# Optimization experiments

Measured on AMD Instinct MI355X. Metric: run time of the kernel, lower is better.

Reference implementation:

```python
import jax, jax.numpy as jnp
import numpy as np

N_HEADS = 8
HEAD_D = 64


def setup_inputs() -> dict:
    key = jax.random.key(0)
    ks = jax.random.split(key, 7)
    b, ds, dc = 4, 4096, 256
    ls, lc = 512, 512
    inner = N_HEADS * HEAD_D  # 512
    out_dim = 512
    data = jax.random.normal(ks[0], (b, ds, dc), dtype=jnp.float32)
    latent = jax.random.normal(ks[1], (b, ls, lc), dtype=jnp.float32)
    # torch nn.Linear weights are [out_features, in_features]
    Wq = jax.random.normal(ks[2], (inner, lc), dtype=jnp.float32) * (lc ** -0.5)
    Wk = jax.random.normal(ks[3], (inner, dc), dtype=jnp.float32) * (dc ** -0.5)
    Wv = jax.random.normal(ks[4], (inner, dc), dtype=jnp.float32) * (dc ** -0.5)
    Wo = jax.random.normal(ks[5], (out_dim, inner), dtype=jnp.float32) * (inner ** -0.5)
    bo = jax.random.normal(ks[6], (out_dim,), dtype=jnp.float32) * 0.02
    return {"data": data, "latent": latent, "Wq": Wq, "Wk": Wk, "Wv": Wv, "Wo": Wo, "bo": bo}


def reference(data, latent, Wq, Wk, Wv, Wo, bo):
    b, ds, _ = data.shape
    ls = latent.shape[1]
    scale = HEAD_D ** -0.5
    # projections, split into heads
    Q = (latent @ Wq.T).reshape(b, ls, N_HEADS, HEAD_D)  # [b,ls,h,d]
    K = (data @ Wk.T).reshape(b, ds, N_HEADS, HEAD_D)    # [b,ds,h,d]
    V = (data @ Wv.T).reshape(b, ds, N_HEADS, HEAD_D)
    # logits [b, ds, ls, h]; original broadcasts then sums over head_d -> einsum
    logits = jnp.einsum('blhd,bshd->bslh', Q, K) * scale
    # softmax over key axis (dim 1 = ds), matching attn_logits.softmax(1)
    attn = jax.nn.softmax(logits, axis=1)
    # weighted sum over keys: [b, ls, h, d] -> [b, ls, inner]
    out = jnp.einsum('bshd,bslh->blhd', V, attn).reshape(b, ls, N_HEADS * HEAD_D)
    # output Linear (dropout is identity in eval)
    return out @ Wo.T + bo
```

## Files before the change

kernel.cpp:

```cpp
#include <hip/hip_runtime.h>

typedef __bf16 bf16;
typedef __bf16 bf16x8 __attribute__((ext_vector_type(8)));
typedef float  f32x4  __attribute__((ext_vector_type(4)));


__device__ __forceinline__ bf16x8 cvt8(float4 a, float4 b) {
    bf16x8 r;
    r[0] = (bf16)a.x; r[1] = (bf16)a.y; r[2] = (bf16)a.z; r[3] = (bf16)a.w;
    r[4] = (bf16)b.x; r[5] = (bf16)b.y; r[6] = (bf16)b.z; r[7] = (bf16)b.w;
    return r;
}

#define LDT 136
__global__ __launch_bounds__(256) void proj_kvq(
    const float* __restrict__ data, const float* __restrict__ latent,
    const float* __restrict__ Wk, const float* __restrict__ Wv, const float* __restrict__ Wq,
    bf16* __restrict__ K_b, bf16* __restrict__ Vt_b, bf16* __restrict__ Q_b)
{
    __shared__ __align__(16) bf16 arena[128 * LDT];

    const int bx = blockIdx.x;
    const int tid = threadIdx.x;
    const int wave = tid >> 6, lane = tid & 63;
    const int wm = wave >> 1, wn = wave & 1;
    const int l15 = lane & 15, quad = lane >> 4;
    const int rowA = tid >> 2;
    const int c8 = (tid & 3) * 8;

    if (bx >= 64) {
        const int t = bx - 64;
        const int m0 = (t & 127) * 128, n0 = (t >> 7) * 128;
        bf16* As  = arena;
        bf16* Bks = arena + 4096;
        bf16* Bvs = arena + 8192;

        const float* Ar0 = data + (size_t)(m0 + rowA) * 256 + c8;
        const float* Ar1 = Ar0 + 64 * 256;
        const float* Kr0 = Wk + (size_t)(n0 + rowA) * 256 + c8;
        const float* Kr1 = Kr0 + 64 * 256;
        const float* Vr0 = Wv + (size_t)(n0 + rowA) * 256 + c8;
        const float* Vr1 = Vr0 + 64 * 256;

        f32x4 accK[4][4] = {}, accV[4][4] = {};
        float4 a00,a01,a10,a11, k00,k01,k10,k11, v00,v01,v10,v11;

#define LOADF(k) do { \
        a00 = *(const float4*)(Ar0 + (k)); a01 = *(const float4*)(Ar0 + (k) + 4); \
        a10 = *(const float4*)(Ar1 + (k)); a11 = *(const float4*)(Ar1 + (k) + 4); \
        k00 = *(const float4*)(Kr0 + (k)); k01 = *(const float4*)(Kr0 + (k) + 4); \
        k10 = *(const float4*)(Kr1 + (k)); k11 = *(const float4*)(Kr1 + (k) + 4); \
        v00 = *(const float4*)(Vr0 + (k)); v01 = *(const float4*)(Vr0 + (k) + 4); \
        v10 = *(const float4*)(Vr1 + (k)); v11 = *(const float4*)(Vr1 + (k) + 4); \
    } while (0)

        LOADF(0);
        for (int k0 = 0; k0 < 256; k0 += 32) {
            __syncthreads();
            *(bf16x8*)(As + (size_t)tid * 8)         = cvt8(a00, a01);
            *(bf16x8*)(As + 2048 + (size_t)tid * 8)  = cvt8(a10, a11);
            *(bf16x8*)(Bks + (size_t)tid * 8)        = cvt8(k00, k01);
            *(bf16x8*)(Bks + 2048 + (size_t)tid * 8) = cvt8(k10, k11);
            *(bf16x8*)(Bvs + (size_t)tid * 8)        = cvt8(v00, v01);
            *(bf16x8*)(Bvs + 2048 + (size_t)tid * 8) = cvt8(v10, v11);
            if (k0 + 32 < 256) LOADF(k0 + 32);
            __syncthreads();

            bf16x8 af[4];
            #pragma unroll
            for (int mt = 0; mt < 4; mt++)
                af[mt] = *(const bf16x8*)(As + (wm * 64 + mt * 16 + l15) * 32 + quad * 8);
            #pragma unroll
            for (int nt = 0; nt < 4; nt++) {
                bf16x8 bk = *(const bf16x8*)(Bks + (wn * 64 + nt * 16 + l15) * 32 + quad * 8);
                #pragma unroll
                for (int mt = 0; mt < 4; mt++)
                    accK[mt][nt] = __builtin_amdgcn_mfma_f32_16x16x32_bf16(af[mt], bk, accK[mt][nt], 0, 0, 0);
            }
            #pragma unroll
            for (int nt = 0; nt < 4; nt++) {
                bf16x8 bv = *(const bf16x8*)(Bvs + (wn * 64 + nt * 16 + l15) * 32 + quad * 8);
                #pragma unroll
                for (int mt = 0; mt < 4; mt++)
                    accV[mt][nt] = __builtin_amdgcn_mfma_f32_16x16x32_bf16(af[mt], bv, accV[mt][nt], 0, 0, 0);
            }
        }
#undef LOADF

        __syncthreads();
        #pragma unroll
        for (int mt = 0; mt < 4; mt++)
            #pragma unroll
            for (int nt = 0; nt < 4; nt++)
                #pragma unroll
                for (int r = 0; r < 4; r++) {
                    int ml = wm * 64 + mt * 16 + quad * 4 + r;
                    int nl = wn * 64 + nt * 16 + l15;
                    arena[ml * LDT + nl] = (bf16)accK[mt][nt][r];
                }
        __syncthreads();
        #pragma unroll
        for (int c = 0; c < 8; c++) {
            int idx = c * 256 + tid;
            int row = idx >> 4, col = (idx & 15) * 8;
            bf16x8 vv = *(const bf16x8*)(arena + row * LDT + col);
            int m = m0 + row, n = n0 + col;
            *(bf16x8*)(K_b + (size_t)((m >> 12) * 8 + (n >> 6)) * 262144 + (m & 4095) * 64 + (n & 63)) = vv;
        }
        __syncthreads();
        #pragma unroll
        for (int mt = 0; mt < 4; mt++)
            #pragma unroll
            for (int nt = 0; nt < 4; nt++)
                #pragma unroll
                for (int r = 0; r < 4; r++) {
                    int ml = wm * 64 + mt * 16 + quad * 4 + r;
                    int nl = wn * 64 + nt * 16 + l15;
                    arena[nl * LDT + ml] = (bf16)accV[mt][nt][r];
                }
        __syncthreads();
        #pragma unroll
        for (int c = 0; c < 8; c++) {
            int idx = c * 256 + tid;
            int row = idx >> 4, col = (idx & 15) * 8;
            bf16x8 vv = *(const bf16x8*)(arena + row * LDT + col);
            int d = n0 + row, s = m0 + col;
            *(bf16x8*)(Vt_b + (size_t)((s >> 12) * 8 + (d >> 6)) * 262144 + (d & 63) * 4096 + (s & 4095)) = vv;
        }
    } else {
        const int m0 = (bx & 15) * 128, n0 = (bx >> 4) * 128;
        bf16* As = arena;
        bf16* Bs = arena + 4096;

        const float* Ar0 = latent + (size_t)(m0 + rowA) * 512 + c8;
        const float* Ar1 = Ar0 + 64 * 512;
        const float* Br0 = Wq + (size_t)(n0 + rowA) * 512 + c8;
        const float* Br1 = Br0 + 64 * 512;

        f32x4 acc[4][4] = {};
        float4 a00, a01, a10, a11, b00, b01, b10, b11;

#define LOADQ(k) do { \
        a00 = *(const float4*)(Ar0 + (k));  a01 = *(const float4*)(Ar0 + (k) + 4); \
        a10 = *(const float4*)(Ar1 + (k));  a11 = *(const float4*)(Ar1 + (k) + 4); \
        b00 = *(const float4*)(Br0 + (k));  b01 = *(const float4*)(Br0 + (k) + 4); \
        b10 = *(const float4*)(Br1 + (k));  b11 = *(const float4*)(Br1 + (k) + 4); \
    } while (0)

        LOADQ(0);
        for (int k0 = 0; k0 < 512; k0 += 32) {
            __syncthreads();
            *(bf16x8*)(As + (size_t)tid * 8)        = cvt8(a00, a01);
            *(bf16x8*)(As + 2048 + (size_t)tid * 8) = cvt8(a10, a11);
            *(bf16x8*)(Bs + (size_t)tid * 8)        = cvt8(b00, b01);
            *(bf16x8*)(Bs + 2048 + (size_t)tid * 8) = cvt8(b10, b11);
            if (k0 + 32 < 512) LOADQ(k0 + 32);
            __syncthreads();

            bf16x8 af[4], bfr[4];
            #pragma unroll
            for (int mt = 0; mt < 4; mt++)
                af[mt] = *(const bf16x8*)(As + (wm * 64 + mt * 16 + l15) * 32 + quad * 8);
            #pragma unroll
            for (int nt = 0; nt < 4; nt++)
                bfr[nt] = *(const bf16x8*)(Bs + (wn * 64 + nt * 16 + l15) * 32 + quad * 8);
            #pragma unroll
            for (int mt = 0; mt < 4; mt++)
                #pragma unroll
                for (int nt = 0; nt < 4; nt++)
                    acc[mt][nt] = __builtin_amdgcn_mfma_f32_16x16x32_bf16(af[mt], bfr[nt], acc[mt][nt], 0, 0, 0);
        }
#undef LOADQ

        __syncthreads();
        #pragma unroll
        for (int mt = 0; mt < 4; mt++)
            #pragma unroll
            for (int nt = 0; nt < 4; nt++)
                #pragma unroll
                for (int r = 0; r < 4; r++) {
                    int ml = wm * 64 + mt * 16 + quad * 4 + r;
                    int nl = wn * 64 + nt * 16 + l15;
                    arena[ml * LDT + nl] = (bf16)acc[mt][nt][r];
                }
        __syncthreads();
        #pragma unroll
        for (int c = 0; c < 8; c++) {
            int idx = c * 256 + tid;
            int row = idx >> 4, col = (idx & 15) * 8;
            bf16x8 vv = *(const bf16x8*)(arena + row * LDT + col);
            int m = m0 + row, n = n0 + col;
            *(bf16x8*)(Q_b + (size_t)((m >> 9) * 8 + (n >> 6)) * 32768 + (m & 511) * 64 + (n & 63)) = vv;
        }
    }
}

#define LDK 72
__global__ __launch_bounds__(256) void flash_attn(
    const bf16* __restrict__ Q, const bf16* __restrict__ K,
    const bf16* __restrict__ Vt, float* __restrict__ Opart, float* __restrict__ lbuf)
{
    __shared__ bf16 Ks[64 * LDK];
    __shared__ bf16 Vs[64 * LDK];
    __shared__ bf16 Ps[4][16 * LDK];

    const int tid = threadIdx.x;
    const int bx = blockIdx.x;
    const int qt = bx >> 7;
    const int bh = (bx & 127) >> 2;
    const int ks = bx & 3;
    const int wave = tid >> 6, lane = tid & 63;
    const int l15 = lane & 15, quad = lane >> 4;

    const bf16* Qb = Q + (size_t)bh * 32768 + (size_t)(qt * 64 + wave * 16 + l15) * 64;
    bf16x8 aq[2];
    aq[0] = *(const bf16x8*)(Qb + quad * 8);
    aq[1] = *(const bf16x8*)(Qb + 32 + quad * 8);

    const bf16* Kb = K + (size_t)bh * 262144;
    const bf16* Vb = Vt + (size_t)bh * 262144;

    f32x4 oacc[4] = {};
    float lpart[4] = {0.f, 0.f, 0.f, 0.f};
    const float scale = 0.125f;

    const int i0 = tid, i1 = tid + 256;
    const int r0 = i0 >> 3, c0 = (i0 & 7) * 8;
    const int r1 = i1 >> 3, c1 = (i1 & 7) * 8;

    const int kstart = ks * 1024, kend = kstart + 1024;

    uint4 pk0 = *(const uint4*)(Kb + (size_t)(kstart + r0) * 64 + c0);
    uint4 pk1 = *(const uint4*)(Kb + (size_t)(kstart + r1) * 64 + c1);
    uint4 pv0 = *(const uint4*)(Vb + (size_t)r0 * 4096 + kstart + c0);
    uint4 pv1 = *(const uint4*)(Vb + (size_t)r1 * 4096 + kstart + c1);

    for (int key0 = kstart; key0 < kend; key0 += 64) {
        __syncthreads();
        *(uint4*)(Ks + r0 * LDK + c0) = pk0;
        *(uint4*)(Ks + r1 * LDK + c1) = pk1;
        *(uint4*)(Vs + r0 * LDK + c0) = pv0;
        *(uint4*)(Vs + r1 * LDK + c1) = pv1;
        if (key0 + 64 < kend) {
            pk0 = *(const uint4*)(Kb + (size_t)(key0 + 64 + r0) * 64 + c0);
            pk1 = *(const uint4*)(Kb + (size_t)(key0 + 64 + r1) * 64 + c1);
            pv0 = *(const uint4*)(Vb + (size_t)r0 * 4096 + key0 + 64 + c0);
            pv1 = *(const uint4*)(Vb + (size_t)r1 * 4096 + key0 + 64 + c1);
        }
        __syncthreads();

        float p[4][4];
        __builtin_amdgcn_s_setprio(1);
        #pragma unroll
        for (int nt = 0; nt < 4; nt++) {
            f32x4 z = {};
            #pragma unroll
            for (int kf = 0; kf < 2; kf++) {
                bf16x8 bk = *(const bf16x8*)(Ks + (nt * 16 + l15) * LDK + kf * 32 + quad * 8);
                z = __builtin_amdgcn_mfma_f32_16x16x32_bf16(aq[kf], bk, z, 0, 0, 0);
            }
            #pragma unroll
            for (int r = 0; r < 4; r++) {
                float e = __expf(z[r] * scale);
                p[r][nt] = e;
                lpart[r] += e;
            }
        }
        __builtin_amdgcn_s_setprio(0);

        #pragma unroll
        for (int r = 0; r < 4; r++)
            #pragma unroll
            for (int nt = 0; nt < 4; nt++)
                Ps[wave][(quad * 4 + r) * LDK + nt * 16 + l15] = (bf16)p[r][nt];

        bf16x8 ap[2];
        ap[0] = *(const bf16x8*)(&Ps[wave][l15 * LDK + quad * 8]);
        ap[1] = *(const bf16x8*)(&Ps[wave][l15 * LDK + 32 + quad * 8]);
        __builtin_amdgcn_s_setprio(1);
        #pragma unroll
        for (int dt = 0; dt < 4; dt++) {
            #pragma unroll
            for (int kf = 0; kf < 2; kf++) {
                bf16x8 bv = *(const bf16x8*)(Vs + (dt * 16 + l15) * LDK + kf * 32 + quad * 8);
                oacc[dt] = __builtin_amdgcn_mfma_f32_16x16x32_bf16(ap[kf], bv, oacc[dt], 0, 0, 0);
            }
        }
        __builtin_amdgcn_s_setprio(0);
    }

    #pragma unroll
    for (int r = 0; r < 4; r++) {
        #pragma unroll
        for (int off = 1; off < 16; off <<= 1) lpart[r] += __shfl_xor(lpart[r], off, 64);
    }

    const int rowbase = bh * 512 + qt * 64 + wave * 16 + quad * 4;
    #pragma unroll
    for (int dt = 0; dt < 4; dt++) {
        #pragma unroll
        for (int r = 0; r < 4; r++) {
            Opart[((size_t)ks * 16384 + rowbase + r) * 64 + dt * 16 + l15] = oacc[dt][r];
        }
    }
    if (l15 == 0) {
        #pragma unroll
        for (int r = 0; r < 4; r++)
            lbuf[(size_t)ks * 16384 + rowbase + r] = lpart[r];
    }
}

__global__ __launch_bounds__(256) void gemm_out(
    const float* __restrict__ Opart, const float* __restrict__ lbuf,
    const float* __restrict__ Wo, const float* __restrict__ bo, float* __restrict__ out)
{
    __shared__ bf16 As[64 * 32];
    __shared__ bf16 Bs[64 * 32];
    const int tid = threadIdx.x;
    const int m0 = blockIdx.x * 64, n0 = blockIdx.y * 64;
    const int wave = tid >> 6, lane = tid & 63;
    const int wm = wave >> 1, wn = wave & 1;
    const int l15 = lane & 15, quad = lane >> 4;
    const int rowA = tid >> 2;
    const int c8 = (tid & 3) * 8;
    const int m = m0 + rowA;
    const int mhi = (m >> 9) << 3, mlo = m & 511;

    f32x4 acc[2][2] = {};
    float4 pa[8]; float pl[4]; float4 pb0, pb1;

    auto loadA = [&](int k0) {
        int kc = k0 + c8;
        int arow = (mhi + (kc >> 6)) * 512 + mlo;
        int d0 = kc & 63;
        #pragma unroll
        for (int ks = 0; ks < 4; ks++) {
            pl[ks] = lbuf[(size_t)ks * 16384 + arow];
            pa[2 * ks]     = *(const float4*)(Opart + ((size_t)ks * 16384 + arow) * 64 + d0);
            pa[2 * ks + 1] = *(const float4*)(Opart + ((size_t)ks * 16384 + arow) * 64 + d0 + 4);
        }
    };
    auto loadB = [&](int k0) {
        pb0 = *(const float4*)(Wo + (size_t)(n0 + rowA) * 512 + k0 + c8);
        pb1 = *(const float4*)(Wo + (size_t)(n0 + rowA) * 512 + k0 + c8 + 4);
    };

    loadA(0); loadB(0);

    for (int k0 = 0; k0 < 512; k0 += 32) {
        __syncthreads();
        {
            float L = pl[0] + pl[1] + pl[2] + pl[3];
            float inv = 1.0f / L;
            float4 s0, s1;
            s0.x = pa[0].x + pa[2].x + pa[4].x + pa[6].x;
            s0.y = pa[0].y + pa[2].y + pa[4].y + pa[6].y;
            s0.z = pa[0].z + pa[2].z + pa[4].z + pa[6].z;
            s0.w = pa[0].w + pa[2].w + pa[4].w + pa[6].w;
            s1.x = pa[1].x + pa[3].x + pa[5].x + pa[7].x;
            s1.y = pa[1].y + pa[3].y + pa[5].y + pa[7].y;
            s1.z = pa[1].z + pa[3].z + pa[5].z + pa[7].z;
            s1.w = pa[1].w + pa[3].w + pa[5].w + pa[7].w;
            s0.x *= inv; s0.y *= inv; s0.z *= inv; s0.w *= inv;
            s1.x *= inv; s1.y *= inv; s1.z *= inv; s1.w *= inv;
            *(bf16x8*)(As + (size_t)tid * 8) = cvt8(s0, s1);
            *(bf16x8*)(Bs + (size_t)tid * 8) = cvt8(pb0, pb1);
        }
        if (k0 + 32 < 512) { loadA(k0 + 32); loadB(k0 + 32); }
        __syncthreads();

        bf16x8 af[2], bfr[2];
        #pragma unroll
        for (int mt = 0; mt < 2; mt++)
            af[mt] = *(const bf16x8*)(As + (wm * 32 + mt * 16 + l15) * 32 + quad * 8);
        #pragma unroll
        for (int nt = 0; nt < 2; nt++)
            bfr[nt] = *(const bf16x8*)(Bs + (wn * 32 + nt * 16 + l15) * 32 + quad * 8);
        #pragma unroll
        for (int mt = 0; mt < 2; mt++)
            #pragma unroll
            for (int nt = 0; nt < 2; nt++)
                acc[mt][nt] = __builtin_amdgcn_mfma_f32_16x16x32_bf16(af[mt], bfr[nt], acc[mt][nt], 0, 0, 0);
    }

    #pragma unroll
    for (int mt = 0; mt < 2; mt++) {
        #pragma unroll
        for (int nt = 0; nt < 2; nt++) {
            #pragma unroll
            for (int r = 0; r < 4; r++) {
                int mm = m0 + wm * 32 + mt * 16 + quad * 4 + r;
                int nn = n0 + wn * 32 + nt * 16 + l15;
                out[(size_t)mm * 512 + nn] = acc[mt][nt][r] + bo[nn];
            }
        }
    }
}

extern "C" void kernel_launch(void* const* d_in, const int* in_sizes, int n_in,
                              void* d_out, int out_size, void* d_ws, size_t ws_size,
                              hipStream_t stream) {
    const float* data   = (const float*)d_in[0];
    const float* latent = (const float*)d_in[1];
    const float* Wq = (const float*)d_in[2];
    const float* Wk = (const float*)d_in[3];
    const float* Wv = (const float*)d_in[4];
    const float* Wo = (const float*)d_in[5];
    const float* bo = (const float*)d_in[6];
    float* out = (float*)d_out;

    bf16* ws = (bf16*)d_ws;
    bf16* Q_b    = ws;
    bf16* K_b    = Q_b + 1048576;
    bf16* Vt_b   = K_b + 8388608;
    float* Opart = (float*)(Vt_b + 8388608);
    float* lbuf  = Opart + 4 * 16384 * 64;

    proj_kvq<<<576, 256, 0, stream>>>(data, latent, Wk, Wv, Wq, K_b, Vt_b, Q_b);
    flash_attn<<<1024, 256, 0, stream>>>(Q_b, K_b, Vt_b, Opart, lbuf);
    gemm_out<<<dim3(32, 8), 256, 0, stream>>>(Opart, lbuf, Wo, bo, out);
}
```

Before: 153.8 us.

## Process two query tiles per wave in flash attention and fold scale into Q

Each wave now handles 32 query rows instead of 16, so every K/V tile loaded into shared memory is reused across twice as many queries and the grid is halved to 512 blocks. The QK^T product is computed transposed (K as A operand), which allows packed bf16x4 writes of P and a cheaper row-sum reduction. The softmax scale is folded into the Q projection epilogue, removing a multiply per logit. The cost is higher register pressure and fewer blocks, which may reduce occupancy and latency hiding.

```diff
diff --git a/kernel.cpp b/kernel.cpp
--- a/kernel.cpp
+++ b/kernel.cpp
@@ -1,6 +1,7 @@
 #include <hip/hip_runtime.h>
 
 typedef __bf16 bf16;
+typedef __bf16 bf16x4 __attribute__((ext_vector_type(4)));
 typedef __bf16 bf16x8 __attribute__((ext_vector_type(8)));
 typedef float  f32x4  __attribute__((ext_vector_type(4)));
 
@@ -181,7 +182,7 @@
                 for (int r = 0; r < 4; r++) {
                     int ml = wm * 64 + mt * 16 + quad * 4 + r;
                     int nl = wn * 64 + nt * 16 + l15;
-                    arena[ml * LDT + nl] = (bf16)acc[mt][nt][r];
+                    arena[ml * LDT + nl] = (bf16)(acc[mt][nt][r] * 0.125f);
                 }
         __syncthreads();
         #pragma unroll
@@ -196,13 +197,14 @@
 }
 
 #define LDK 72
+#define LDP 72
 __global__ __launch_bounds__(256) void flash_attn(
     const bf16* __restrict__ Q, const bf16* __restrict__ K,
     const bf16* __restrict__ Vt, float* __restrict__ Opart, float* __restrict__ lbuf)
 {
     __shared__ bf16 Ks[64 * LDK];
     __shared__ bf16 Vs[64 * LDK];
-    __shared__ bf16 Ps[4][16 * LDK];
+    __shared__ bf16 Ps[4][2 * 16 * LDP];
 
     const int tid = threadIdx.x;
     const int bx = blockIdx.x;
@@ -212,17 +214,18 @@
     const int wave = tid >> 6, lane = tid & 63;
     const int l15 = lane & 15, quad = lane >> 4;
 
-    const bf16* Qb = Q + (size_t)bh * 32768 + (size_t)(qt * 64 + wave * 16 + l15) * 64;
-    bf16x8 aq[2];
-    aq[0] = *(const bf16x8*)(Qb + quad * 8);
-    aq[1] = *(const bf16x8*)(Qb + 32 + quad * 8);
+    const bf16* Qb = Q + (size_t)bh * 32768 + (size_t)(qt * 128 + wave * 32 + l15) * 64;
+    bf16x8 aq[2][2];
+    aq[0][0] = *(const bf16x8*)(Qb + quad * 8);
+    aq[0][1] = *(const bf16x8*)(Qb + 32 + quad * 8);
+    aq[1][0] = *(const bf16x8*)(Qb + 1024 + quad * 8);
+    aq[1][1] = *(const bf16x8*)(Qb + 1024 + 32 + quad * 8);
 
     const bf16* Kb = K + (size_t)bh * 262144;
     const bf16* Vb = Vt + (size_t)bh * 262144;
 
-    f32x4 oacc[4] = {};
-    float lpart[4] = {0.f, 0.f, 0.f, 0.f};
-    const float scale = 0.125f;
+    f32x4 oacc[2][4] = {};
+    float lsum[2] = {0.f, 0.f};
 
     const int i0 = tid, i1 = tid + 256;
     const int r0 = i0 >> 3, c0 = (i0 & 7) * 8;
@@ -234,6 +237,8 @@
     uint4 pk1 = *(const uint4*)(Kb + (size_t)(kstart + r1) * 64 + c1);
     uint4 pv0 = *(const uint4*)(Vb + (size_t)r0 * 4096 + kstart + c0);
     uint4 pv1 = *(const uint4*)(Vb + (size_t)r1 * 4096 + kstart + c1);
+
+    bf16* Pw = &Ps[wave][0];
 
     for (int key0 = kstart; key0 < kend; key0 += 64) {
         __syncthreads();
@@ -249,64 +254,69 @@
         }
         __syncthreads();
 
-        float p[4][4];
         __builtin_amdgcn_s_setprio(1);
         #pragma unroll
-        for (int nt = 0; nt < 4; nt++) {
-            f32x4 z = {};
-            #pragma unroll
-            for (int kf = 0; kf < 2; kf++) {
-                bf16x8 bk = *(const bf16x8*)(Ks + (nt * 16 + l15) * LDK + kf * 32 + quad * 8);
-                z = __builtin_amdgcn_mfma_f32_16x16x32_bf16(aq[kf], bk, z, 0, 0, 0);
-            }
+        for (int mt = 0; mt < 4; mt++) {
+            bf16x8 bk0 = *(const bf16x8*)(Ks + (mt * 16 + l15) * LDK + quad * 8);
+            bf16x8 bk1 = *(const bf16x8*)(Ks + (mt * 16 + l15) * LDK + 32 + quad * 8);
+            #pragma unroll
+            for (int u = 0; u < 2; u++) {
+                f32x4 z = {};
+                z = __builtin_amdgcn_mfma_f32_16x16x32_bf16(bk0, aq[u][0], z, 0, 0, 0);
+                z = __builtin_amdgcn_mfma_f32_16x16x32_bf16(bk1, aq[u][1], z, 0, 0, 0);
+                bf16x4 pv4;
+                float s = 0.f;
+                #pragma unroll
+                for (int r = 0; r < 4; r++) {
+                    float e = __expf(z[r]);
+                    s += e;
+                    pv4[r] = (bf16)e;
+                }
+                lsum[u] += s;
+                *(bf16x4*)(Pw + u * 16 * LDP + l15 * LDP + mt * 16 + quad * 4) = pv4;
+            }
+        }
+        __builtin_amdgcn_s_setprio(0);
+
+        bf16x8 ap[2][2];
+        #pragma unroll
+        for (int u = 0; u < 2; u++) {
+            ap[u][0] = *(const bf16x8*)(Pw + u * 16 * LDP + l15 * LDP + quad * 8);
+            ap[u][1] = *(const bf16x8*)(Pw + u * 16 * LDP + l15 * LDP + 32 + quad * 8);
+        }
+        __builtin_amdgcn_s_setprio(1);
+        #pragma unroll
+        for (int dt = 0; dt < 4; dt++) {
+            bf16x8 bv0 = *(const bf16x8*)(Vs + (dt * 16 + l15) * LDK + quad * 8);
+            bf16x8 bv1 = *(const bf16x8*)(Vs + (dt * 16 + l15) * LDK + 32 + quad * 8);
+            #pragma unroll
+            for (int u = 0; u < 2; u++) {
+                oacc[u][dt] = __builtin_amdgcn_mfma_f32_16x16x32_bf16(ap[u][0], bv0, oacc[u][dt], 0, 0, 0);
+                oacc[u][dt] = __builtin_amdgcn_mfma_f32_16x16x32_bf16(ap[u][1], bv1, oacc[u][dt], 0, 0, 0);
+            }
+        }
+        __builtin_amdgcn_s_setprio(0);
+    }
+
+    #pragma unroll
+    for (int u = 0; u < 2; u++) {
+        lsum[u] += __shfl_xor(lsum[u], 16, 64);
+        lsum[u] += __shfl_xor(lsum[u], 32, 64);
+    }
+
+    #pragma unroll
+    for (int u = 0; u < 2; u++) {
+        const int rowbase = bh * 512 + qt * 128 + wave * 32 + u * 16 + quad * 4;
+        #pragma unroll
+        for (int dt = 0; dt < 4; dt++) {
             #pragma unroll
             for (int r = 0; r < 4; r++) {
-                float e = __expf(z[r] * scale);
-                p[r][nt] = e;
-                lpart[r] += e;
-            }
-        }
-        __builtin_amdgcn_s_setprio(0);
-
-        #pragma unroll
-        for (int r = 0; r < 4; r++)
-            #pragma unroll
-            for (int nt = 0; nt < 4; nt++)
-                Ps[wave][(quad * 4 + r) * LDK + nt * 16 + l15] = (bf16)p[r][nt];
-
-        bf16x8 ap[2];
-        ap[0] = *(const bf16x8*)(&Ps[wave][l15 * LDK + quad * 8]);
-        ap[1] = *(const bf16x8*)(&Ps[wave][l15 * LDK + 32 + quad * 8]);
-        __builtin_amdgcn_s_setprio(1);
-        #pragma unroll
-        for (int dt = 0; dt < 4; dt++) {
-            #pragma unroll
-            for (int kf = 0; kf < 2; kf++) {
-                bf16x8 bv = *(const bf16x8*)(Vs + (dt * 16 + l15) * LDK + kf * 32 + quad * 8);
-                oacc[dt] = __builtin_amdgcn_mfma_f32_16x16x32_bf16(ap[kf], bv, oacc[dt], 0, 0, 0);
-            }
-        }
-        __builtin_amdgcn_s_setprio(0);
-    }
-
-    #pragma unroll
-    for (int r = 0; r < 4; r++) {
-        #pragma unroll
-        for (int off = 1; off < 16; off <<= 1) lpart[r] += __shfl_xor(lpart[r], off, 64);
-    }
-
-    const int rowbase = bh * 512 + qt * 64 + wave * 16 + quad * 4;
-    #pragma unroll
-    for (int dt = 0; dt < 4; dt++) {
-        #pragma unroll
-        for (int r = 0; r < 4; r++) {
-            Opart[((size_t)ks * 16384 + rowbase + r) * 64 + dt * 16 + l15] = oacc[dt][r];
-        }
-    }
-    if (l15 == 0) {
-        #pragma unroll
-        for (int r = 0; r < 4; r++)
-            lbuf[(size_t)ks * 16384 + rowbase + r] = lpart[r];
+                Opart[((size_t)ks * 16384 + rowbase + r) * 64 + dt * 16 + l15] = oacc[u][dt][r];
+            }
+        }
+        if (quad == 0) {
+            lbuf[(size_t)ks * 16384 + bh * 512 + qt * 128 + wave * 32 + u * 16 + l15] = lsum[u];
+        }
     }
 }
 
@@ -417,6 +427,6 @@
     float* lbuf  = Opart + 4 * 16384 * 64;
 
     proj_kvq<<<576, 256, 0, stream>>>(data, latent, Wk, Wv, Wq, K_b, Vt_b, Q_b);
-    flash_attn<<<1024, 256, 0, stream>>>(Q_b, K_b, Vt_b, Opart, lbuf);
+    flash_attn<<<512, 256, 0, stream>>>(Q_b, K_b, Vt_b, Opart, lbuf);
     gemm_out<<<dim3(32, 8), 256, 0, stream>>>(Opart, lbuf, Wo, bo, out);
 }
```

Result: faster. 149.1 us (-3.1%).
